# Performance work log

Hardware: AMD Instinct MI355X
Metric: run time of the kernel (lower is better)

## Reference

```python
import jax, jax.numpy as jnp
import numpy as np

TOP_K = 2

def setup_inputs() -> dict:
    key = jax.random.key(0)
    ks = jax.random.split(key, 5)
    B, T, C, E, H = 4, 2048, 1024, 16, 4096
    x = jax.random.normal(ks[0], (B, T, C), dtype=jnp.float32)
    w_router = jax.random.normal(ks[1], (C, E), dtype=jnp.float32) / np.sqrt(C)
    w1 = jax.random.normal(ks[2], (E, C, H), dtype=jnp.float32) / np.sqrt(C)
    b1 = jnp.zeros((E, H), dtype=jnp.float32)
    w2 = jax.random.normal(ks[3], (E, H, C), dtype=jnp.float32) / np.sqrt(H)
    b2 = jnp.zeros((E, C), dtype=jnp.float32)
    return {"x": x, "w_router": w_router, "w1": w1, "b1": b1, "w2": w2, "b2": b2}


def reference(x, w_router, w1, b1, w2, b2):
    B, T, C = x.shape
    E = w1.shape[0]
    xf = x.reshape(-1, C)                       # [N, C]
    N = xf.shape[0]

    logits = xf @ w_router                      # [N, E]
    rw, sel = jax.lax.top_k(logits, TOP_K)      # [N, K]
    rw = jax.nn.softmax(rw.astype(jnp.float32), axis=-1).astype(x.dtype)

    # combine weight per (token, expert): sum of routing weights over the
    # k-slots that selected that expert (equivalent to the per-k masked loop)
    comb = jnp.zeros((N, E), dtype=x.dtype)
    comb = comb.at[jnp.arange(N)[:, None], sel].add(rw)  # [N, E]

    # loop over experts via scan: out += comb[:, e:e+1] * FFN_e(xf)
    def step(acc, params):
        w1e, b1e, w2e, b2e, ce = params         # ce: [N]
        h = jax.nn.relu(xf @ w1e + b1e)         # [N, 4C]
        y = h @ w2e + b2e                       # [N, C]
        return acc + ce[:, None] * y, None

    out0 = jnp.zeros_like(xf)
    out, _ = jax.lax.scan(step, out0, (w1, b1, w2, b2, comb.T))
    return out.reshape(B, T, C)
```

## Files before the change

kernel.cpp:

```cpp
#include <hip/hip_runtime.h>
#include <hip/hip_bf16.h>


typedef __attribute__((ext_vector_type(4))) float f32x4;
typedef __attribute__((ext_vector_type(8))) __bf16 bf16x8;
typedef __attribute__((ext_vector_type(8))) unsigned short u16x8;

#define NEXP 16
#define CAP  2048
#define CDIM 1024
#define HDIM 4096
#define KS2 2
#define BMG 256
#define BNG 256
#define SLOT 8192

__device__ __forceinline__ unsigned short f2bf(float f) {
  return __builtin_bit_cast(unsigned short, (__bf16)f);
}

__device__ __forceinline__ void xcd_remap(int& bx, int& by, int& bz) {
  const int gx = gridDim.x, gy = gridDim.y;
  const int nwg = gx * gy * gridDim.z;
  int flat = blockIdx.x + gx * (blockIdx.y + gy * blockIdx.z);
  flat = (flat & 7) * (nwg >> 3) + (flat >> 3);
  bx = flat % gx;
  const int t = flat / gx;
  by = t % gy;
  bz = t / gy;
}

__global__ __launch_bounds__(64) void router_kernel(
    const float* __restrict__ x, const float* __restrict__ wr,
    float* __restrict__ pair_w, int* __restrict__ counts,
    int* __restrict__ lists, unsigned short* __restrict__ xb)
{
  const int n = blockIdx.x;
  const int l = threadIdx.x;
  const float* xrow = x + (size_t)n * CDIM;
  unsigned short* xbrow = xb + (size_t)n * CDIM;
  double acc[NEXP];
#pragma unroll
  for (int e = 0; e < NEXP; e++) acc[e] = 0.0;
  for (int it = 0; it < CDIM / 64; it++) {
    const int c = l + it * 64;
    const float xf = xrow[c];
    xbrow[c] = f2bf(xf);
    const double xv = (double)xf;
    const float* w = wr + c * NEXP;
#pragma unroll
    for (int e = 0; e < NEXP; e++) acc[e] += xv * (double)w[e];
  }
#pragma unroll
  for (int e = 0; e < NEXP; e++) {
    double v = acc[e];
    for (int off = 32; off > 0; off >>= 1) v += __shfl_xor(v, off, 64);
    acc[e] = v;
  }
  if (l == 0) {
    int e0 = 0; double b0 = acc[0];
    for (int e = 1; e < NEXP; e++) if (acc[e] > b0) { b0 = acc[e]; e0 = e; }
    int e1 = -1; double b1v = -1e300;
    for (int e = 0; e < NEXP; e++) {
      if (e == e0) continue;
      if (acc[e] > b1v) { b1v = acc[e]; e1 = e; }
    }
    const double d = exp(b1v - b0);
    pair_w[2 * n]     = (float)(1.0 / (1.0 + d));
    pair_w[2 * n + 1] = (float)(d / (1.0 + d));
    int p0 = atomicAdd(&counts[e0], 1);
    if (p0 < CAP) lists[e0 * CAP + p0] = 2 * n;
    int p1 = atomicAdd(&counts[e1], 1);
    if (p1 < CAP) lists[e1 * CAP + p1] = 2 * n + 1;
  }
}


#define LOADA(kbyte)                                                           \
  do {                                                                         \
    rA0 = *(const u16x8*)(ag0 + (kbyte));                                      \
    rA1 = *(const u16x8*)(ag1 + (kbyte));                                      \
    rA2 = *(const u16x8*)(ag0 + (kbyte) + 64);                                 \
    rA3 = *(const u16x8*)(ag1 + (kbyte) + 64);                                 \
  } while (0)

#define DSWA(parx)                                                             \
  do {                                                                         \
    unsigned short* S0_ = &lds[((parx) * 2 + 0) * SLOT];                       \
    unsigned short* S1_ = &lds[((parx) * 2 + 1) * SLOT];                       \
    *(u16x8*)(S0_ + sw0) = rA0;                                                \
    *(u16x8*)(S0_ + sw1) = rA1;                                                \
    *(u16x8*)(S1_ + sw0) = rA2;                                                \
    *(u16x8*)(S1_ + sw1) = rA3;                                                \
  } while (0)

#define LOADB(ktv)                                                             \
  do {                                                                         \
    _Pragma("unroll")                                                          \
    for (int u = 0; u < 4; u++)                                                \
      _Pragma("unroll")                                                        \
      for (int j = 0; j < 8; j++)                                              \
        rB[u][j] = bgu[u][(size_t)((ktv) + j) * BNN];                          \
  } while (0)

#define DSWB(parx)                                                             \
  do {                                                                         \
    unsigned short* SB_ = &lds[4 * SLOT + ((parx) * 2 + bh) * SLOT];           \
    _Pragma("unroll")                                                          \
    for (int u = 0; u < 4; u++) {                                              \
      u16x8 v_;                                                                \
      _Pragma("unroll")                                                        \
      for (int j = 0; j < 8; j++) v_[j] = f2bf(rB[u][j]);                      \
      *(u16x8*)(SB_ + brow * 32 + (u ^ bqx) * 8) = v_;                         \
    }                                                                          \
  } while (0)

#define COMPUTE(parx, hx)                                                      \
  do {                                                                         \
    const unsigned short* As_ = &lds[((parx) * 2 + (hx)) * SLOT];              \
    const unsigned short* Bs_ = &lds[4 * SLOT + ((parx) * 2 + (hx)) * SLOT];   \
    bf16x8 af[8], bfv[4];                                                      \
    _Pragma("unroll")                                                          \
    for (int mf = 0; mf < 8; mf++)                                             \
      af[mf] = *(const bf16x8*)(As_ + (wr * 128 + mf * 16 + lrow) * 32 + qsw); \
    _Pragma("unroll")                                                          \
    for (int nf = 0; nf < 4; nf++)                                             \
      bfv[nf] = *(const bf16x8*)(Bs_ + (wc * 64 + nf * 16 + lrow) * 32 + qsw); \
    __builtin_amdgcn_s_setprio(1);                                             \
    _Pragma("unroll")                                                          \
    for (int mf = 0; mf < 8; mf++)                                             \
      _Pragma("unroll")                                                        \
      for (int nf = 0; nf < 4; nf++)                                           \
        acc[mf][nf] = __builtin_amdgcn_mfma_f32_16x16x32_bf16(                 \
            af[mf], bfv[nf], acc[mf][nf], 0, 0, 0);                            \
    __builtin_amdgcn_s_setprio(0);                                             \
  } while (0)

#define SBAR asm volatile("s_barrier" ::: "memory")

#define GEMM_MAIN_LOOP(NT)                                                     \
  u16x8 rA0, rA1, rA2, rA3; float rB[4][8];                                    \
  LOADA(0); LOADB(0);                                                          \
  DSWA(0); DSWB(0);                                                            \
  LOADA(128); LOADB(64);                                                       \
  asm volatile("s_waitcnt lgkmcnt(0)" ::: "memory");                           \
  for (int tt = 0; tt < (NT); ++tt) {                                          \
    const int par = tt & 1;                                                    \
    SBAR;                                                                      \
    if (tt + 1 < (NT)) { DSWA(par ^ 1); DSWB(par ^ 1); }                       \
    if (tt + 2 < (NT)) { LOADA((tt + 2) * 128); LOADB((tt + 2) * 64); }        \
    COMPUTE(par, 0);                                                           \
    COMPUTE(par, 1);                                                           \
  }

__global__ __launch_bounds__(512, 2) void gemm1_8p_kernel(
    const unsigned short* __restrict__ xb, const float* __restrict__ w1f,
    const float* __restrict__ b1, const int* __restrict__ counts,
    const int* __restrict__ lists, unsigned short* __restrict__ Hb)
{
  int bx, by, bz;
  xcd_remap(bx, by, bz);
  const int e = bz;
  int cnt = counts[e]; if (cnt > CAP) cnt = CAP;
  const int m0 = by * BMG;
  if (m0 >= cnt) return;
  const int n0 = bx * BNG;
  const int* list = lists + e * CAP;
  const float* Wf = w1f + (size_t)e * CDIM * HDIM;
  const int BNN = HDIM;

  __shared__ __align__(16) unsigned short lds[8 * SLOT];

  const int t = threadIdx.x, w = t >> 6, lane = t & 63;
  const int wr = w >> 2, wc = w & 3;
  const int lrow = lane & 15, lgrp = lane >> 4;
  const int qsw = (lgrp ^ ((lrow >> 1) & 3)) * 8;

  const int sr0 = w * 16 + (lane >> 2), sr1 = 128 + sr0;
  const int wq = ((lane & 3) ^ ((lane >> 3) & 3)) * 8;
  const int sw0 = sr0 * 32 + wq, sw1 = sr1 * 32 + wq;
  int ai0 = m0 + sr0; if (ai0 > cnt - 1) ai0 = cnt - 1;
  int ai1 = m0 + sr1; if (ai1 > cnt - 1) ai1 = cnt - 1;
  const char* ag0 = (const char*)(xb + (size_t)(list[ai0] >> 1) * CDIM) + (lane & 3) * 16;
  const char* ag1 = (const char*)(xb + (size_t)(list[ai1] >> 1) * CDIM) + (lane & 3) * 16;

  const int brow = t & 255, bh = t >> 8, bqx = (brow >> 1) & 3;
  const float* bgu[4];
#pragma unroll
  for (int u = 0; u < 4; u++)
    bgu[u] = Wf + (size_t)(bh * 32 + u * 8) * BNN + n0 + brow;

  f32x4 acc[8][4] = {};

  GEMM_MAIN_LOOP(CDIM / 64)

  int hrow[8][4]; bool valid[8][4];
#pragma unroll
  for (int mf = 0; mf < 8; mf++)
#pragma unroll
    for (int rr = 0; rr < 4; rr++) {
      const int mi = m0 + wr * 128 + mf * 16 + lgrp * 4 + rr;
      valid[mf][rr] = (mi < cnt);
      hrow[mf][rr] = list[valid[mf][rr] ? mi : (cnt - 1)];
    }
#pragma unroll
  for (int nf = 0; nf < 4; nf++) {
    const int col = n0 + wc * 64 + nf * 16 + lrow;
    const float bias = b1[e * HDIM + col];
#pragma unroll
    for (int mf = 0; mf < 8; mf++)
#pragma unroll
      for (int rr = 0; rr < 4; rr++)
        if (valid[mf][rr]) {
          float h = acc[mf][nf][rr] + bias;
          h = h > 0.f ? h : 0.f;
          Hb[(size_t)hrow[mf][rr] * HDIM + col] = f2bf(h);
        }
  }
}

__global__ __launch_bounds__(512, 2) void gemm2_8p_kernel(
    const unsigned short* __restrict__ Hb, const float* __restrict__ w2f,
    const float* __restrict__ b2, const float* __restrict__ pair_w,
    const int* __restrict__ counts, const int* __restrict__ lists,
    float* __restrict__ out)
{
  int bx, by, bz;
  xcd_remap(bx, by, bz);
  const int e = bz / KS2, ks = bz % KS2;
  int cnt = counts[e]; if (cnt > CAP) cnt = CAP;
  const int m0 = by * BMG;
  if (m0 >= cnt) return;
  const int n0 = bx * BNG;
  const int* list = lists + e * CAP;
  const float* Wf = w2f + (size_t)e * HDIM * CDIM;
  const int BNN = CDIM;
  const int kbeg = ks * (HDIM / KS2);

  __shared__ __align__(16) unsigned short lds[8 * SLOT];

  const int t = threadIdx.x, w = t >> 6, lane = t & 63;
  const int wr = w >> 2, wc = w & 3;
  const int lrow = lane & 15, lgrp = lane >> 4;
  const int qsw = (lgrp ^ ((lrow >> 1) & 3)) * 8;

  const int sr0 = w * 16 + (lane >> 2), sr1 = 128 + sr0;
  const int wq = ((lane & 3) ^ ((lane >> 3) & 3)) * 8;
  const int sw0 = sr0 * 32 + wq, sw1 = sr1 * 32 + wq;
  int ai0 = m0 + sr0; if (ai0 > cnt - 1) ai0 = cnt - 1;
  int ai1 = m0 + sr1; if (ai1 > cnt - 1) ai1 = cnt - 1;
  const char* ag0 = (const char*)(Hb + (size_t)list[ai0] * HDIM + kbeg) + (lane & 3) * 16;
  const char* ag1 = (const char*)(Hb + (size_t)list[ai1] * HDIM + kbeg) + (lane & 3) * 16;

  const int brow = t & 255, bh = t >> 8, bqx = (brow >> 1) & 3;
  const float* bgu[4];
#pragma unroll
  for (int u = 0; u < 4; u++)
    bgu[u] = Wf + (size_t)(kbeg + bh * 32 + u * 8) * BNN + n0 + brow;

  f32x4 acc[8][4] = {};

  GEMM_MAIN_LOOP((HDIM / KS2) / 64)

  float wgt[8][4]; int tok[8][4]; bool valid[8][4];
#pragma unroll
  for (int mf = 0; mf < 8; mf++)
#pragma unroll
    for (int rr = 0; rr < 4; rr++) {
      const int mi = m0 + wr * 128 + mf * 16 + lgrp * 4 + rr;
      valid[mf][rr] = (mi < cnt);
      const int p = list[valid[mf][rr] ? mi : (cnt - 1)];
      wgt[mf][rr] = pair_w[p];
      tok[mf][rr] = p >> 1;
    }
#pragma unroll
  for (int nf = 0; nf < 4; nf++) {
    const int col = n0 + wc * 64 + nf * 16 + lrow;
    const float bias = (ks == 0) ? b2[e * CDIM + col] : 0.f;
#pragma unroll
    for (int mf = 0; mf < 8; mf++)
#pragma unroll
      for (int rr = 0; rr < 4; rr++)
        if (valid[mf][rr])
          atomicAdd(out + (size_t)tok[mf][rr] * CDIM + col,
                    wgt[mf][rr] * (acc[mf][nf][rr] + bias));
  }
}

__device__ __forceinline__ int swz(int row, int b) {
  return row * 128 + (b ^ (((row >> 1) & 7) << 4));
}

#define MFMA_COMPUTE_F(Abase, Bbase)                                           \
  _Pragma("unroll")                                                            \
  for (int kk = 0; kk < 2; kk++) {                                             \
    bf16x8 af[4], bfr[4];                                                      \
    const int kb = (kk * 32 + lgrp * 8) * 2;                                   \
    _Pragma("unroll")                                                          \
    for (int i = 0; i < 4; i++)                                                \
      af[i] = *(const bf16x8*)((Abase) + swz(wm + i * 16 + lrow, kb));         \
    _Pragma("unroll")                                                          \
    for (int j = 0; j < 4; j++)                                                \
      bfr[j] = *(const bf16x8*)((Bbase) + swz(wn + j * 16 + lrow, kb));        \
    _Pragma("unroll")                                                          \
    for (int i = 0; i < 4; i++)                                                \
      _Pragma("unroll")                                                        \
      for (int j = 0; j < 4; j++)                                              \
        acc[i][j] = __builtin_amdgcn_mfma_f32_16x16x32_bf16(                   \
            af[i], bfr[j], acc[i][j], 0, 0, 0);                                \
  }

__global__ __launch_bounds__(256) void gemm1_f32_kernel(
    const float* __restrict__ x, const float* __restrict__ w1,
    const float* __restrict__ b1, const int* __restrict__ counts,
    const int* __restrict__ lists, unsigned short* __restrict__ Hb,
    int e_base, int h_by_pair)
{
  const int e = e_base + blockIdx.z;
  int cnt = counts[e]; if (cnt > CAP) cnt = CAP;
  const int m0 = blockIdx.y * 128;
  if (m0 >= cnt) return;
  const int n0 = blockIdx.x * 128;
  const int* list = lists + e * CAP;
  const float* W = w1 + (size_t)e * CDIM * HDIM;
  __shared__ __align__(16) unsigned short As[128 * 64];
  __shared__ __align__(16) unsigned short Bs[128 * 64];
  const int t = threadIdx.x;
  const int a_row = t >> 1, a_half = t & 1;
  int a_idx = m0 + a_row; if (a_idx > cnt - 1) a_idx = cnt - 1;
  const float* a_src = x + (size_t)(list[a_idx] >> 1) * CDIM + a_half * 32;
  const int b_np = t & 63, b_kg = t >> 6;
  const int wid = t >> 6, lane = t & 63;
  const int wm = (wid >> 1) * 64, wn = (wid & 1) * 64;
  const int lrow = lane & 15, lgrp = lane >> 4;
  f32x4 acc[4][4] = {};
  for (int kt = 0; kt < CDIM; kt += 64) {
    {
      const float* s = a_src + kt;
      u16x8 cv[4];
#pragma unroll
      for (int q = 0; q < 4; q++) {
        float4 v0 = *(const float4*)(s + q * 8);
        float4 v1 = *(const float4*)(s + q * 8 + 4);
        cv[q][0] = f2bf(v0.x); cv[q][1] = f2bf(v0.y);
        cv[q][2] = f2bf(v0.z); cv[q][3] = f2bf(v0.w);
        cv[q][4] = f2bf(v1.x); cv[q][5] = f2bf(v1.y);
        cv[q][6] = f2bf(v1.z); cv[q][7] = f2bf(v1.w);
      }
#pragma unroll
      for (int q = 0; q < 4; q++)
        *(u16x8*)((char*)As + swz(a_row, (a_half * 32 + q * 8) * 2)) = cv[q];
    }
    {
#pragma unroll
      for (int it = 0; it < 2; it++) {
        const int k0 = (b_kg + 4 * it) * 8;
        u16x8 c0, c1;
#pragma unroll
        for (int j = 0; j < 8; j++) {
          float2 v = *(const float2*)(W + (size_t)(kt + k0 + j) * HDIM + n0 + 2 * b_np);
          c0[j] = f2bf(v.x); c1[j] = f2bf(v.y);
        }
        *(u16x8*)((char*)Bs + swz(2 * b_np,     k0 * 2)) = c0;
        *(u16x8*)((char*)Bs + swz(2 * b_np + 1, k0 * 2)) = c1;
      }
    }
    __syncthreads();
    MFMA_COMPUTE_F((const char*)As, (const char*)Bs)
    __syncthreads();
  }
  int hrow[4][4]; bool valid[4][4];
#pragma unroll
  for (int i = 0; i < 4; i++)
#pragma unroll
    for (int r = 0; r < 4; r++) {
      const int mi = m0 + wm + i * 16 + lgrp * 4 + r;
      valid[i][r] = (mi < cnt);
      const int idx = valid[i][r] ? mi : (cnt - 1);
      hrow[i][r] = h_by_pair ? list[idx] : idx;
    }
#pragma unroll
  for (int j = 0; j < 4; j++) {
    const int col = n0 + wn + j * 16 + lrow;
    const float bias = b1[e * HDIM + col];
#pragma unroll
    for (int i = 0; i < 4; i++)
#pragma unroll
      for (int r = 0; r < 4; r++)
        if (valid[i][r]) {
          float h = acc[i][j][r] + bias;
          h = h > 0.f ? h : 0.f;
          Hb[(size_t)hrow[i][r] * HDIM + col] = f2bf(h);
        }
  }
}

__global__ __launch_bounds__(256) void gemm2_f32_kernel(
    const unsigned short* __restrict__ Hb, const float* __restrict__ w2,
    const float* __restrict__ b2, const float* __restrict__ pair_w,
    const int* __restrict__ counts, const int* __restrict__ lists,
    float* __restrict__ out, int e_base, int h_by_pair)
{
  const int e = e_base + blockIdx.z;
  int cnt = counts[e]; if (cnt > CAP) cnt = CAP;
  const int m0 = blockIdx.y * 128;
  if (m0 >= cnt) return;
  const int n0 = blockIdx.x * 128;
  const int* list = lists + e * CAP;
  const float* W = w2 + (size_t)e * HDIM * CDIM;
  __shared__ __align__(16) unsigned short As[128 * 64];
  __shared__ __align__(16) unsigned short Bs[128 * 64];
  const int t = threadIdx.x;
  const int a_row = t >> 1, a_half = t & 1;
  int a_idx = m0 + a_row; if (a_idx > cnt - 1) a_idx = cnt - 1;
  const unsigned short* a_src =
      Hb + (size_t)(h_by_pair ? list[a_idx] : a_idx) * HDIM + a_half * 32;
  const int b_np = t & 63, b_kg = t >> 6;
  const int wid = t >> 6, lane = t & 63;
  const int wm = (wid >> 1) * 64, wn = (wid & 1) * 64;
  const int lrow = lane & 15, lgrp = lane >> 4;
  f32x4 acc[4][4] = {};
  for (int kt = 0; kt < HDIM; kt += 64) {
    {
      const unsigned short* s = a_src + kt;
#pragma unroll
      for (int q = 0; q < 4; q++) {
        u16x8 v = *(const u16x8*)(s + q * 8);
        *(u16x8*)((char*)As + swz(a_row, (a_half * 32 + q * 8) * 2)) = v;
      }
    }
    {
#pragma unroll
      for (int it = 0; it < 2; it++) {
        const int k0 = (b_kg + 4 * it) * 8;
        u16x8 c0, c1;
#pragma unroll
        for (int j = 0; j < 8; j++) {
          float2 v = *(const float2*)(W + (size_t)(kt + k0 + j) * CDIM + n0 + 2 * b_np);
          c0[j] = f2bf(v.x); c1[j] = f2bf(v.y);
        }
        *(u16x8*)((char*)Bs + swz(2 * b_np,     k0 * 2)) = c0;
        *(u16x8*)((char*)Bs + swz(2 * b_np + 1, k0 * 2)) = c1;
      }
    }
    __syncthreads();
    MFMA_COMPUTE_F((const char*)As, (const char*)Bs)
    __syncthreads();
  }
  float wgt[4][4]; int tok[4][4]; bool valid[4][4];
#pragma unroll
  for (int i = 0; i < 4; i++)
#pragma unroll
    for (int r = 0; r < 4; r++) {
      const int mi = m0 + wm + i * 16 + lgrp * 4 + r;
      valid[i][r] = (mi < cnt);
      const int idx = valid[i][r] ? mi : (cnt - 1);
      const int p = list[idx];
      wgt[i][r] = pair_w[p];
      tok[i][r] = p >> 1;
    }
#pragma unroll
  for (int j = 0; j < 4; j++) {
    const int col = n0 + wn + j * 16 + lrow;
    const float bias = b2[e * CDIM + col];
#pragma unroll
    for (int i = 0; i < 4; i++)
#pragma unroll
      for (int r = 0; r < 4; r++)
        if (valid[i][r])
          atomicAdd(out + (size_t)tok[i][r] * CDIM + col,
                    wgt[i][r] * (acc[i][j][r] + bias));
  }
}

extern "C" void kernel_launch(void* const* d_in, const int* in_sizes, int n_in,
                              void* d_out, int out_size, void* d_ws, size_t ws_size,
                              hipStream_t stream)
{
  const float* x  = (const float*)d_in[0];
  const float* wr = (const float*)d_in[1];
  const float* w1 = (const float*)d_in[2];
  const float* b1 = (const float*)d_in[3];
  const float* w2 = (const float*)d_in[4];
  const float* b2 = (const float*)d_in[5];
  float* out = (float*)d_out;

  const int N = in_sizes[0] / CDIM;

  char* ws = (char*)d_ws;
  int* counts = (int*)ws;
  int* lists  = (int*)(ws + 256);
  float* pw   = (float*)(ws + 256 + NEXP * CAP * 4);
  size_t off = 256 + (size_t)NEXP * CAP * 4 + (size_t)2 * N * 4;
  off = (off + 255) & ~(size_t)255;
  unsigned short* xb = (unsigned short*)(ws + off);
  const size_t xb_sz = (size_t)N * CDIM * 2;
  unsigned short* Hb = (unsigned short*)(ws + off + xb_sz);
  const size_t Hb_sz = (size_t)2 * N * HDIM * 2;

  const size_t need_new = off + xb_sz + Hb_sz;
  const size_t need_old = off + Hb_sz;

  hipMemsetAsync(d_ws, 0, 64, stream);
  hipMemsetAsync(d_out, 0, (size_t)out_size * 4, stream);

  if (ws_size >= need_new) {
    router_kernel<<<N, 64, 0, stream>>>(x, wr, pw, counts, lists, xb);
    gemm1_8p_kernel<<<dim3(HDIM / BNG, CAP / BMG, NEXP), 512, 0, stream>>>(
        xb, w1, b1, counts, lists, Hb);
    gemm2_8p_kernel<<<dim3(CDIM / BNG, CAP / BMG, NEXP * KS2), 512, 0, stream>>>(
        Hb, w2, b2, pw, counts, lists, out);
  } else if (ws_size >= need_old) {
    unsigned short* Hb0 = (unsigned short*)(ws + off);
    router_kernel<<<N, 64, 0, stream>>>(x, wr, pw, counts, lists, Hb0);
    gemm1_f32_kernel<<<dim3(HDIM / 128, CAP / 128, NEXP), 256, 0, stream>>>(
        x, w1, b1, counts, lists, Hb0, 0, 1);
    gemm2_f32_kernel<<<dim3(CDIM / 128, CAP / 128, NEXP), 256, 0, stream>>>(
        Hb0, w2, b2, pw, counts, lists, out, 0, 1);
  }
}
```

Baseline: 876.7 us.

## Shrink MoE expert GEMM tiles to 128x128 with 256-thread blocks and K=32 stages

Replaces the 256x256-tile, 512-thread grouped GEMM kernels with 128x128 tiles, 4 waves, 32-deep K stages and a simpler double-buffered LDS pipeline, at 3 blocks per CU. The router is also changed to process four tokens per 256-thread block. Smaller tiles give more blocks and better load balance across uneven expert counts. In exchange they cut operand reuse, so more fp32 weight traffic must be read and converted per FLOP, and the pipeline takes more barriers per K.

```diff
diff --git a/kernel.cpp b/kernel.cpp
--- a/kernel.cpp
+++ b/kernel.cpp
@@ -11,9 +11,7 @@
 #define CDIM 1024
 #define HDIM 4096
 #define KS2 2
-#define BMG 256
-#define BNG 256
-#define SLOT 8192
+#define SLOTE (128 * 32)
 
 __device__ __forceinline__ unsigned short f2bf(float f) {
   return __builtin_bit_cast(unsigned short, (__bf16)f);
@@ -30,13 +28,13 @@
   bz = t / gy;
 }
 
-__global__ __launch_bounds__(64) void router_kernel(
+__global__ __launch_bounds__(256) void router_kernel(
     const float* __restrict__ x, const float* __restrict__ wr,
     float* __restrict__ pair_w, int* __restrict__ counts,
     int* __restrict__ lists, unsigned short* __restrict__ xb)
 {
-  const int n = blockIdx.x;
-  const int l = threadIdx.x;
+  const int n = blockIdx.x * 4 + (threadIdx.x >> 6);
+  const int l = threadIdx.x & 63;
   const float* xrow = x + (size_t)n * CDIM;
   unsigned short* xbrow = xb + (size_t)n * CDIM;
   double acc[NEXP];
@@ -76,59 +74,46 @@
 }
 
 
-#define LOADA(kbyte)                                                           \
+#define LOADA(sb)                                                              \
   do {                                                                         \
-    rA0 = *(const u16x8*)(ag0 + (kbyte));                                      \
-    rA1 = *(const u16x8*)(ag1 + (kbyte));                                      \
-    rA2 = *(const u16x8*)(ag0 + (kbyte) + 64);                                 \
-    rA3 = *(const u16x8*)(ag1 + (kbyte) + 64);                                 \
+    rA0 = *(const u16x8*)(agA + (sb));                                         \
+    rA1 = *(const u16x8*)(agA + (sb) + 16);                                    \
   } while (0)
 
-#define DSWA(parx)                                                             \
+#define LOADB(sk)                                                              \
   do {                                                                         \
-    unsigned short* S0_ = &lds[((parx) * 2 + 0) * SLOT];                       \
-    unsigned short* S1_ = &lds[((parx) * 2 + 1) * SLOT];                       \
-    *(u16x8*)(S0_ + sw0) = rA0;                                                \
-    *(u16x8*)(S0_ + sw1) = rA1;                                                \
-    *(u16x8*)(S1_ + sw0) = rA2;                                                \
-    *(u16x8*)(S1_ + sw1) = rA3;                                                \
+    _Pragma("unroll")                                                          \
+    for (int j = 0; j < 16; j++)                                               \
+      rB[j] = bgB[(size_t)((sk) + j) * BNN];                                   \
   } while (0)
 
-#define LOADB(ktv)                                                             \
+#define DSW(parx)                                                              \
   do {                                                                         \
-    _Pragma("unroll")                                                          \
-    for (int u = 0; u < 4; u++)                                                \
-      _Pragma("unroll")                                                        \
-      for (int j = 0; j < 8; j++)                                              \
-        rB[u][j] = bgu[u][(size_t)((ktv) + j) * BNN];                          \
+    unsigned short* SA_ = &lds[(parx) * SLOTE];                                \
+    unsigned short* SB_ = &lds[2 * SLOTE + (parx) * SLOTE];                    \
+    *(u16x8*)(SA_ + swA0) = rA0;                                               \
+    *(u16x8*)(SA_ + swA1) = rA1;                                               \
+    u16x8 v0_, v1_;                                                            \
+    _Pragma("unroll")                                                          \
+    for (int i = 0; i < 8; i++) { v0_[i] = f2bf(rB[i]); v1_[i] = f2bf(rB[8 + i]); } \
+    *(u16x8*)(SB_ + swB0) = v0_;                                               \
+    *(u16x8*)(SB_ + swB1) = v1_;                                               \
   } while (0)
 
-#define DSWB(parx)                                                             \
+#define COMPUTE(parx)                                                          \
   do {                                                                         \
-    unsigned short* SB_ = &lds[4 * SLOT + ((parx) * 2 + bh) * SLOT];           \
-    _Pragma("unroll")                                                          \
-    for (int u = 0; u < 4; u++) {                                              \
-      u16x8 v_;                                                                \
-      _Pragma("unroll")                                                        \
-      for (int j = 0; j < 8; j++) v_[j] = f2bf(rB[u][j]);                      \
-      *(u16x8*)(SB_ + brow * 32 + (u ^ bqx) * 8) = v_;                         \
-    }                                                                          \
-  } while (0)
-
-#define COMPUTE(parx, hx)                                                      \
-  do {                                                                         \
-    const unsigned short* As_ = &lds[((parx) * 2 + (hx)) * SLOT];              \
-    const unsigned short* Bs_ = &lds[4 * SLOT + ((parx) * 2 + (hx)) * SLOT];   \
-    bf16x8 af[8], bfv[4];                                                      \
-    _Pragma("unroll")                                                          \
-    for (int mf = 0; mf < 8; mf++)                                             \
-      af[mf] = *(const bf16x8*)(As_ + (wr * 128 + mf * 16 + lrow) * 32 + qsw); \
+    const unsigned short* As_ = &lds[(parx) * SLOTE];                          \
+    const unsigned short* Bs_ = &lds[2 * SLOTE + (parx) * SLOTE];              \
+    bf16x8 af[4], bfv[4];                                                      \
+    _Pragma("unroll")                                                          \
+    for (int mf = 0; mf < 4; mf++)                                             \
+      af[mf] = *(const bf16x8*)(As_ + (wm + mf * 16 + lrow) * 32 + qsw);       \
     _Pragma("unroll")                                                          \
     for (int nf = 0; nf < 4; nf++)                                             \
-      bfv[nf] = *(const bf16x8*)(Bs_ + (wc * 64 + nf * 16 + lrow) * 32 + qsw); \
+      bfv[nf] = *(const bf16x8*)(Bs_ + (wn + nf * 16 + lrow) * 32 + qsw);      \
     __builtin_amdgcn_s_setprio(1);                                             \
     _Pragma("unroll")                                                          \
-    for (int mf = 0; mf < 8; mf++)                                             \
+    for (int mf = 0; mf < 4; mf++)                                             \
       _Pragma("unroll")                                                        \
       for (int nf = 0; nf < 4; nf++)                                           \
         acc[mf][nf] = __builtin_amdgcn_mfma_f32_16x16x32_bf16(                 \
@@ -136,24 +121,23 @@
     __builtin_amdgcn_s_setprio(0);                                             \
   } while (0)
 
-#define SBAR asm volatile("s_barrier" ::: "memory")
-
-#define GEMM_MAIN_LOOP(NT)                                                     \
-  u16x8 rA0, rA1, rA2, rA3; float rB[4][8];                                    \
+#define LGKM0 asm volatile("s_waitcnt lgkmcnt(0)" ::: "memory")
+#define SBAR  asm volatile("s_barrier" ::: "memory")
+
+#define GEMM_MAIN_LOOP(NS)                                                     \
+  u16x8 rA0, rA1; float rB[16];                                                \
   LOADA(0); LOADB(0);                                                          \
-  DSWA(0); DSWB(0);                                                            \
-  LOADA(128); LOADB(64);                                                       \
-  asm volatile("s_waitcnt lgkmcnt(0)" ::: "memory");                           \
-  for (int tt = 0; tt < (NT); ++tt) {                                          \
-    const int par = tt & 1;                                                    \
-    SBAR;                                                                      \
-    if (tt + 1 < (NT)) { DSWA(par ^ 1); DSWB(par ^ 1); }                       \
-    if (tt + 2 < (NT)) { LOADA((tt + 2) * 128); LOADB((tt + 2) * 64); }        \
-    COMPUTE(par, 0);                                                           \
-    COMPUTE(par, 1);                                                           \
-  }
-
-__global__ __launch_bounds__(512, 2) void gemm1_8p_kernel(
+  DSW(0);                                                                      \
+  LOADA(64); LOADB(32);                                                        \
+  for (int s = 0; s < (NS); ++s) {                                             \
+    const int par = s & 1;                                                     \
+    LGKM0; SBAR;                                                               \
+    if (s + 1 < (NS)) DSW(par ^ 1);                                            \
+    if (s + 2 < (NS)) { LOADA((s + 2) * 64); LOADB((s + 2) * 32); }            \
+    COMPUTE(par);                                                              \
+  }
+
+__global__ __launch_bounds__(256, 3) void gemm1_k_kernel(
     const unsigned short* __restrict__ xb, const float* __restrict__ w1f,
     const float* __restrict__ b1, const int* __restrict__ counts,
     const int* __restrict__ lists, unsigned short* __restrict__ Hb)
@@ -162,64 +146,61 @@
   xcd_remap(bx, by, bz);
   const int e = bz;
   int cnt = counts[e]; if (cnt > CAP) cnt = CAP;
-  const int m0 = by * BMG;
+  const int m0 = by * 128;
   if (m0 >= cnt) return;
-  const int n0 = bx * BNG;
+  const int n0 = bx * 128;
   const int* list = lists + e * CAP;
   const float* Wf = w1f + (size_t)e * CDIM * HDIM;
   const int BNN = HDIM;
 
-  __shared__ __align__(16) unsigned short lds[8 * SLOT];
-
-  const int t = threadIdx.x, w = t >> 6, lane = t & 63;
-  const int wr = w >> 2, wc = w & 3;
+  __shared__ __align__(16) unsigned short lds[4 * SLOTE];
+
+  const int t = threadIdx.x, wv = t >> 6, lane = t & 63;
+  const int wm = (wv >> 1) * 64, wn = (wv & 1) * 64;
   const int lrow = lane & 15, lgrp = lane >> 4;
   const int qsw = (lgrp ^ ((lrow >> 1) & 3)) * 8;
 
-  const int sr0 = w * 16 + (lane >> 2), sr1 = 128 + sr0;
-  const int wq = ((lane & 3) ^ ((lane >> 3) & 3)) * 8;
-  const int sw0 = sr0 * 32 + wq, sw1 = sr1 * 32 + wq;
-  int ai0 = m0 + sr0; if (ai0 > cnt - 1) ai0 = cnt - 1;
-  int ai1 = m0 + sr1; if (ai1 > cnt - 1) ai1 = cnt - 1;
-  const char* ag0 = (const char*)(xb + (size_t)(list[ai0] >> 1) * CDIM) + (lane & 3) * 16;
-  const char* ag1 = (const char*)(xb + (size_t)(list[ai1] >> 1) * CDIM) + (lane & 3) * 16;
-
-  const int brow = t & 255, bh = t >> 8, bqx = (brow >> 1) & 3;
-  const float* bgu[4];
-#pragma unroll
-  for (int u = 0; u < 4; u++)
-    bgu[u] = Wf + (size_t)(bh * 32 + u * 8) * BNN + n0 + brow;
-
-  f32x4 acc[8][4] = {};
-
-  GEMM_MAIN_LOOP(CDIM / 64)
-
-  int hrow[8][4]; bool valid[8][4];
-#pragma unroll
-  for (int mf = 0; mf < 8; mf++)
-#pragma unroll
-    for (int rr = 0; rr < 4; rr++) {
-      const int mi = m0 + wr * 128 + mf * 16 + lgrp * 4 + rr;
-      valid[mf][rr] = (mi < cnt);
-      hrow[mf][rr] = list[valid[mf][rr] ? mi : (cnt - 1)];
-    }
-#pragma unroll
-  for (int nf = 0; nf < 4; nf++) {
-    const int col = n0 + wc * 64 + nf * 16 + lrow;
+  const int ar = t & 127, ahi = t >> 7, aqx = (ar >> 1) & 3;
+  const int swA0 = ar * 32 + ((2 * ahi) ^ aqx) * 8;
+  const int swA1 = ar * 32 + ((2 * ahi + 1) ^ aqx) * 8;
+  int ai = m0 + ar; if (ai > cnt - 1) ai = cnt - 1;
+  const char* agA = (const char*)(xb + (size_t)(list[ai] >> 1) * CDIM) + ahi * 32;
+
+  const int bn = t & 127, bkh = t >> 7, bqx = (bn >> 1) & 3;
+  const int swB0 = bn * 32 + ((2 * bkh) ^ bqx) * 8;
+  const int swB1 = bn * 32 + ((2 * bkh + 1) ^ bqx) * 8;
+  const float* bgB = Wf + (size_t)(bkh * 16) * BNN + n0 + bn;
+
+  f32x4 acc[4][4] = {};
+
+  GEMM_MAIN_LOOP(CDIM / 32)
+
+  int hrow[4][4]; bool valid[4][4];
+#pragma unroll
+  for (int i = 0; i < 4; i++)
+#pragma unroll
+    for (int r = 0; r < 4; r++) {
+      const int mi = m0 + wm + i * 16 + lgrp * 4 + r;
+      valid[i][r] = (mi < cnt);
+      hrow[i][r] = list[valid[i][r] ? mi : (cnt - 1)];
+    }
+#pragma unroll
+  for (int j = 0; j < 4; j++) {
+    const int col = n0 + wn + j * 16 + lrow;
     const float bias = b1[e * HDIM + col];
 #pragma unroll
-    for (int mf = 0; mf < 8; mf++)
-#pragma unroll
-      for (int rr = 0; rr < 4; rr++)
-        if (valid[mf][rr]) {
-          float h = acc[mf][nf][rr] + bias;
+    for (int i = 0; i < 4; i++)
+#pragma unroll
+      for (int r = 0; r < 4; r++)
+        if (valid[i][r]) {
+          float h = acc[i][j][r] + bias;
           h = h > 0.f ? h : 0.f;
-          Hb[(size_t)hrow[mf][rr] * HDIM + col] = f2bf(h);
+          Hb[(size_t)hrow[i][r] * HDIM + col] = f2bf(h);
         }
   }
 }
 
-__global__ __launch_bounds__(512, 2) void gemm2_8p_kernel(
+__global__ __launch_bounds__(256, 3) void gemm2_k_kernel(
     const unsigned short* __restrict__ Hb, const float* __restrict__ w2f,
     const float* __restrict__ b2, const float* __restrict__ pair_w,
     const int* __restrict__ counts, const int* __restrict__ lists,
@@ -229,61 +210,58 @@
   xcd_remap(bx, by, bz);
   const int e = bz / KS2, ks = bz % KS2;
   int cnt = counts[e]; if (cnt > CAP) cnt = CAP;
-  const int m0 = by * BMG;
+  const int m0 = by * 128;
   if (m0 >= cnt) return;
-  const int n0 = bx * BNG;
+  const int n0 = bx * 128;
   const int* list = lists + e * CAP;
   const float* Wf = w2f + (size_t)e * HDIM * CDIM;
   const int BNN = CDIM;
   const int kbeg = ks * (HDIM / KS2);
 
-  __shared__ __align__(16) unsigned short lds[8 * SLOT];
-
-  const int t = threadIdx.x, w = t >> 6, lane = t & 63;
-  const int wr = w >> 2, wc = w & 3;
+  __shared__ __align__(16) unsigned short lds[4 * SLOTE];
+
+  const int t = threadIdx.x, wv = t >> 6, lane = t & 63;
+  const int wm = (wv >> 1) * 64, wn = (wv & 1) * 64;
   const int lrow = lane & 15, lgrp = lane >> 4;
   const int qsw = (lgrp ^ ((lrow >> 1) & 3)) * 8;
 
-  const int sr0 = w * 16 + (lane >> 2), sr1 = 128 + sr0;
-  const int wq = ((lane & 3) ^ ((lane >> 3) & 3)) * 8;
-  const int sw0 = sr0 * 32 + wq, sw1 = sr1 * 32 + wq;
-  int ai0 = m0 + sr0; if (ai0 > cnt - 1) ai0 = cnt - 1;
-  int ai1 = m0 + sr1; if (ai1 > cnt - 1) ai1 = cnt - 1;
-  const char* ag0 = (const char*)(Hb + (size_t)list[ai0] * HDIM + kbeg) + (lane & 3) * 16;
-  const char* ag1 = (const char*)(Hb + (size_t)list[ai1] * HDIM + kbeg) + (lane & 3) * 16;
-
-  const int brow = t & 255, bh = t >> 8, bqx = (brow >> 1) & 3;
-  const float* bgu[4];
-#pragma unroll
-  for (int u = 0; u < 4; u++)
-    bgu[u] = Wf + (size_t)(kbeg + bh * 32 + u * 8) * BNN + n0 + brow;
-
-  f32x4 acc[8][4] = {};
-
-  GEMM_MAIN_LOOP((HDIM / KS2) / 64)
-
-  float wgt[8][4]; int tok[8][4]; bool valid[8][4];
-#pragma unroll
-  for (int mf = 0; mf < 8; mf++)
-#pragma unroll
-    for (int rr = 0; rr < 4; rr++) {
-      const int mi = m0 + wr * 128 + mf * 16 + lgrp * 4 + rr;
-      valid[mf][rr] = (mi < cnt);
-      const int p = list[valid[mf][rr] ? mi : (cnt - 1)];
-      wgt[mf][rr] = pair_w[p];
-      tok[mf][rr] = p >> 1;
-    }
-#pragma unroll
-  for (int nf = 0; nf < 4; nf++) {
-    const int col = n0 + wc * 64 + nf * 16 + lrow;
+  const int ar = t & 127, ahi = t >> 7, aqx = (ar >> 1) & 3;
+  const int swA0 = ar * 32 + ((2 * ahi) ^ aqx) * 8;
+  const int swA1 = ar * 32 + ((2 * ahi + 1) ^ aqx) * 8;
+  int ai = m0 + ar; if (ai > cnt - 1) ai = cnt - 1;
+  const char* agA = (const char*)(Hb + (size_t)list[ai] * HDIM + kbeg) + ahi * 32;
+
+  const int bn = t & 127, bkh = t >> 7, bqx = (bn >> 1) & 3;
+  const int swB0 = bn * 32 + ((2 * bkh) ^ bqx) * 8;
+  const int swB1 = bn * 32 + ((2 * bkh + 1) ^ bqx) * 8;
+  const float* bgB = Wf + (size_t)(kbeg + bkh * 16) * BNN + n0 + bn;
+
+  f32x4 acc[4][4] = {};
+
+  GEMM_MAIN_LOOP((HDIM / KS2) / 32)
+
+  float wgt[4][4]; int tok[4][4]; bool valid[4][4];
+#pragma unroll
+  for (int i = 0; i < 4; i++)
+#pragma unroll
+    for (int r = 0; r < 4; r++) {
+      const int mi = m0 + wm + i * 16 + lgrp * 4 + r;
+      valid[i][r] = (mi < cnt);
+      const int p = list[valid[i][r] ? mi : (cnt - 1)];
+      wgt[i][r] = pair_w[p];
+      tok[i][r] = p >> 1;
+    }
+#pragma unroll
+  for (int j = 0; j < 4; j++) {
+    const int col = n0 + wn + j * 16 + lrow;
     const float bias = (ks == 0) ? b2[e * CDIM + col] : 0.f;
 #pragma unroll
-    for (int mf = 0; mf < 8; mf++)
-#pragma unroll
-      for (int rr = 0; rr < 4; rr++)
-        if (valid[mf][rr])
-          atomicAdd(out + (size_t)tok[mf][rr] * CDIM + col,
-                    wgt[mf][rr] * (acc[mf][nf][rr] + bias));
+    for (int i = 0; i < 4; i++)
+#pragma unroll
+      for (int r = 0; r < 4; r++)
+        if (valid[i][r])
+          atomicAdd(out + (size_t)tok[i][r] * CDIM + col,
+                    wgt[i][r] * (acc[i][j][r] + bias));
   }
 }
 
@@ -505,14 +483,14 @@
   hipMemsetAsync(d_out, 0, (size_t)out_size * 4, stream);
 
   if (ws_size >= need_new) {
-    router_kernel<<<N, 64, 0, stream>>>(x, wr, pw, counts, lists, xb);
-    gemm1_8p_kernel<<<dim3(HDIM / BNG, CAP / BMG, NEXP), 512, 0, stream>>>(
+    router_kernel<<<N / 4, 256, 0, stream>>>(x, wr, pw, counts, lists, xb);
+    gemm1_k_kernel<<<dim3(HDIM / 128, CAP / 128, NEXP), 256, 0, stream>>>(
         xb, w1, b1, counts, lists, Hb);
-    gemm2_8p_kernel<<<dim3(CDIM / BNG, CAP / BMG, NEXP * KS2), 512, 0, stream>>>(
+    gemm2_k_kernel<<<dim3(CDIM / 128, CAP / 128, NEXP * KS2), 256, 0, stream>>>(
         Hb, w2, b2, pw, counts, lists, out);
   } else if (ws_size >= need_old) {
     unsigned short* Hb0 = (unsigned short*)(ws + off);
-    router_kernel<<<N, 64, 0, stream>>>(x, wr, pw, counts, lists, Hb0);
+    router_kernel<<<N / 4, 256, 0, stream>>>(x, wr, pw, counts, lists, Hb0);
     gemm1_f32_kernel<<<dim3(HDIM / 128, CAP / 128, NEXP), 256, 0, stream>>>(
         x, w1, b1, counts, lists, Hb0, 0, 1);
     gemm2_f32_kernel<<<dim3(CDIM / 128, CAP / 128, NEXP), 256, 0, stream>>>(
```

Result: slower. 1.141 ms (+30.1%).
